# Optimization experiments

Measured on AMD Instinct MI355X. Metric: run time of the kernel, lower is better.

The kernel has to match this reference:

```python
import jax, jax.numpy as jnp
import numpy as np

B, U, D, SKIP = 2048, 1024, 1024, 24

def setup_inputs() -> dict:
    key = jax.random.key(0)
    ks = jax.random.split(key, 8)
    return {
        "inputs": jax.random.normal(ks[0], (B, D), dtype=jnp.float32),
        "h_tm1": jax.random.normal(ks[1], (B, 4 * U), dtype=jnp.float32),
        "c_tm1": jax.random.normal(ks[2], (B, U), dtype=jnp.float32),
        "step": jnp.zeros((B, 1), dtype=jnp.float32),
        "prev_h": jax.random.normal(ks[3], (B, U * SKIP), dtype=jnp.float32),
        "kernel": jax.random.normal(ks[4], (D, 4 * U), dtype=jnp.float32) * (1.0 / np.sqrt(D)),
        "recurrent_kernel": jax.random.normal(ks[5], (U, 4 * U), dtype=jnp.float32) * (1.0 / np.sqrt(U)),
        "kernel2": jax.random.normal(ks[6], (U, U), dtype=jnp.float32) * (1.0 / np.sqrt(U)),
        "bias": jnp.zeros((4 * U,), dtype=jnp.float32),
        "bias2": jnp.zeros((U,), dtype=jnp.float32),
        "s0": jnp.float32(0.5),
    }

def reference(inputs, h_tm1, c_tm1, step, prev_h, kernel, recurrent_kernel, kernel2, bias, bias2, s0):
    units = kernel2.shape[0]
    # split previous 'h' state into its four gate-history blocks [B, U] each
    h_parts = jnp.stack(jnp.split(h_tm1, 4, axis=1), axis=0)          # [4, B, U]
    rk = recurrent_kernel.reshape(units, 4, units)                     # [U, 4, U]
    # fused per-gate recurrent matmuls: r[g] = h_parts[g] @ recurrent_kernel[:, g*U:(g+1)*U]
    r = jnp.einsum('gbu,ugv->gbv', h_parts, rk)                        # [4, B, U]
    x = inputs @ kernel + bias                                         # [B, 4U]
    x_i, x_f, x_c, x_o = jnp.split(x, 4, axis=1)
    i = jax.nn.sigmoid(x_i + r[0])
    f = jax.nn.sigmoid(x_f + r[1])
    c = f * c_tm1 + i * jnp.tanh(x_c + r[2])
    o = jax.nn.sigmoid(x_o + r[3])
    h = o * jnp.tanh(c)
    new_h_skip = jax.nn.sigmoid(prev_h[:, :units] @ kernel2 + bias2)
    h = s0 * h + new_h_skip * (1 - s0)
    new_h_tm1 = jnp.concatenate([i, f, c, o], axis=1)
    new_prev_h = jnp.concatenate([prev_h[:, units:], h], axis=1)
    return (h, new_h_tm1, c, step + 1, new_prev_h)
```

## Files before the change

kernel.cpp:

```cpp
#include <hip/hip_runtime.h>
#include <hip/hip_bf16.h>
#include <stdint.h>

#define BB 2048
#define UU 1024
#define SKIPN 24

typedef __attribute__((ext_vector_type(8))) short short8;
typedef __attribute__((ext_vector_type(4))) float f32x4;
typedef __attribute__((ext_vector_type(4))) unsigned short ushort4_t;

static __device__ __forceinline__ float sigmoidf_(float x) {
    return 1.0f / (1.0f + __expf(-x));
}

static __device__ __forceinline__ void load_lds16(const void* g, void* l) {
    __builtin_amdgcn_global_load_lds((const __attribute__((address_space(1))) void*)g,
                                     (__attribute__((address_space(3))) void*)l, 16, 0, 0);
}

static __device__ __forceinline__ f32x4 ntl(const f32x4* p) {
    return __builtin_nontemporal_load(p);
}
static __device__ __forceinline__ void nts(f32x4* p, f32x4 v) {
    __builtin_nontemporal_store(v, p);
}

__global__ __launch_bounds__(256) void prep(
    const float* __restrict__ inputs, const float* __restrict__ h_tm1,
    const float* __restrict__ prev_h, const float* __restrict__ kernel,
    const float* __restrict__ rkernel, const float* __restrict__ kernel2,
    __hip_bfloat16* __restrict__ kt, __hip_bfloat16* __restrict__ rkt,
    __hip_bfloat16* __restrict__ k2t, __hip_bfloat16* __restrict__ xin,
    __hip_bfloat16* __restrict__ hb, __hip_bfloat16* __restrict__ ph0) {
    const int bid = blockIdx.x;
    if (bid < 9216) {
        __shared__ float tile[32][33];
        const float* src;
        __hip_bfloat16* dst;
        int C, local;
        if (bid < 4096)      { src = kernel;  dst = kt;  C = 4096; local = bid; }
        else if (bid < 8192) { src = rkernel; dst = rkt; C = 4096; local = bid - 4096; }
        else                 { src = kernel2; dst = k2t; C = 1024; local = bid - 8192; }
        const int xt = (C == 4096) ? 128 : 32;
        const int bc = (local % xt) * 32;
        const int br = (local / xt) * 32;
        const int tx = threadIdx.x & 31, ty = threadIdx.x >> 5;
#pragma unroll
        for (int i = 0; i < 32; i += 8)
            tile[ty + i][tx] = src[(size_t)(br + ty + i) * C + bc + tx];
        __syncthreads();
#pragma unroll
        for (int i = 0; i < 32; i += 8)
            dst[(size_t)(bc + ty + i) * 1024 + br + tx] = __float2bfloat16(tile[tx][ty + i]);
    } else {
        const int idx = (bid - 9216) * 256 + threadIdx.x;
        const float* src;
        __hip_bfloat16* dst;
        int off;
        if (idx < 524288) { dst = xin; off = idx; src = inputs + (size_t)off * 4; }
        else if (idx < 2621440) { off = idx - 524288; dst = hb; src = h_tm1 + (size_t)off * 4; }
        else {
            const int i = idx - 2621440;
            const int b = i >> 8, c4 = i & 255;
            off = i; dst = ph0;
            src = prev_h + (size_t)b * (UU * SKIPN) + c4 * 4;
        }
        const float4 v = *(const float4*)src;
        union { __hip_bfloat16 h[4]; ushort4_t u; } cv;
        cv.h[0] = __float2bfloat16(v.x);
        cv.h[1] = __float2bfloat16(v.y);
        cv.h[2] = __float2bfloat16(v.z);
        cv.h[3] = __float2bfloat16(v.w);
        *(ushort4_t*)(dst + (size_t)off * 4) = cv.u;
    }
}

__global__ __launch_bounds__(256) void mega6(
    const __hip_bfloat16* __restrict__ xin,
    const __hip_bfloat16* __restrict__ hb,
    const __hip_bfloat16* __restrict__ ph0,
    const __hip_bfloat16* __restrict__ kt,
    const __hip_bfloat16* __restrict__ rkt,
    const __hip_bfloat16* __restrict__ k2t,
    const float* __restrict__ prev_h, float* __restrict__ out_prev,
    __hip_bfloat16* __restrict__ pre) {
    const int bid = blockIdx.x;
    if (bid >= 640) {
        const int b = bid - 640;
        const f32x4* s = (const f32x4*)(prev_h + (size_t)b * 24576 + 1024);
        f32x4* d = (f32x4*)(out_prev + (size_t)b * 24576);
        int c = threadIdx.x;
#pragma unroll 1
        for (int it = 0; it < 5; ++it) {
            f32x4 v0 = ntl(s + c);
            f32x4 v1 = ntl(s + c + 256);
            f32x4 v2 = ntl(s + c + 512);
            f32x4 v3 = ntl(s + c + 768);
            nts(d + c, v0);
            nts(d + c + 256, v1);
            nts(d + c + 512, v2);
            nts(d + c + 768, v3);
            c += 1024;
        }
        {
            f32x4 v0 = ntl(s + c);
            f32x4 v1 = ntl(s + c + 256);
            f32x4 v2 = ntl(s + c + 512);
            nts(d + c, v0);
            nts(d + c + 256, v1);
            nts(d + c + 512, v2);
        }
        return;
    }
    const int gi = bid;
    const int g = gi % 5;
    const int t = gi / 5;
    const int v0 = (t & 7) * 128;
    const int b0 = (t >> 3) * 128;

    __shared__ char As[3 * 8192];
    __shared__ char Bs[3 * 8192];

    const int tid = threadIdx.x;
    const int lane = tid & 63;
    const int wid = tid >> 6;
    const int wrow = wid >> 1;
    const int wcol = wid & 1;

    const int srow = tid >> 2;
    const int sslot = tid & 3;
    const int kofs = ((sslot ^ (srow & 3) ^ ((srow >> 2) & 3)) << 3);
    const int ldst = wid * 1024;

    const int l15 = lane & 15;
    const int hi = lane >> 4;
    const int rswB = ((hi ^ (l15 & 3) ^ ((l15 >> 2) & 3)) << 4);

    f32x4 acc[4][4];
#pragma unroll
    for (int m = 0; m < 4; m++)
#pragma unroll
        for (int n = 0; n < 4; n++) acc[m][n] = (f32x4){0.f, 0.f, 0.f, 0.f};

    const __hip_bfloat16* A1;
    const __hip_bfloat16* W1;
    const __hip_bfloat16* A2 = nullptr;
    const __hip_bfloat16* W2 = nullptr;
    int lda1;
    if (g < 4) {
        A1 = xin; lda1 = 1024;
        W1 = kt + (size_t)g * 1048576;
        A2 = hb + (size_t)g * 1024;
        W2 = rkt + (size_t)g * 1048576;
    } else {
        A1 = ph0; lda1 = 1024;
        W1 = k2t;
    }

#define BARRIER() asm volatile("s_barrier" ::: "memory")
#define WAITV(N) asm volatile("s_waitcnt vmcnt(" #N ")" ::: "memory")
#define WAITL0() asm volatile("s_waitcnt lgkmcnt(0)" ::: "memory")

#define KSEG(AB, LDA, WB)                                                          \
    {                                                                              \
        const __hip_bfloat16* Ar0 = (AB) + (size_t)(b0 + srow) * (LDA) + kofs;     \
        const __hip_bfloat16* Ar1 = (AB) + (size_t)(b0 + 64 + srow) * (LDA) + kofs;\
        const __hip_bfloat16* Wr0 = (WB) + (size_t)(v0 + srow) * 1024 + kofs;      \
        const __hip_bfloat16* Wr1 = (WB) + (size_t)(v0 + 64 + srow) * 1024 + kofs; \
        load_lds16(Ar0, As + ldst);                                                \
        load_lds16(Ar1, As + ldst + 4096);                                         \
        load_lds16(Wr0, Bs + ldst);                                                \
        load_lds16(Wr1, Bs + ldst + 4096);                                         \
        load_lds16(Ar0 + 32, As + 8192 + ldst);                                    \
        load_lds16(Ar1 + 32, As + 8192 + ldst + 4096);                             \
        load_lds16(Wr0 + 32, Bs + 8192 + ldst);                                    \
        load_lds16(Wr1 + 32, Bs + 8192 + ldst + 4096);                             \
        int cur = 0;                                                               \
        for (int t_ = 0; t_ < 32; ++t_) {                                          \
            char* Ac = As + cur * 8192;                                            \
            char* Bc = Bs + cur * 8192;                                            \
            if (t_ < 30) {                                                         \
                int nxt = cur + 2; if (nxt >= 3) nxt -= 3;                         \
                const int kn = (t_ + 2) * 32;                                      \
                char* An = As + nxt * 8192 + ldst;                                 \
                char* Bn = Bs + nxt * 8192 + ldst;                                 \
                load_lds16(Ar0 + kn, An);                                          \
                load_lds16(Ar1 + kn, An + 4096);                                   \
                load_lds16(Wr0 + kn, Bn);                                          \
                load_lds16(Wr1 + kn, Bn + 4096);                                   \
                WAITV(8);                                                          \
            } else if (t_ == 30) {                                                 \
                WAITV(4);                                                          \
            } else {                                                               \
                WAITV(0);                                                          \
            }                                                                      \
            BARRIER();                                                             \
            short8 af[4], bfr[4];                                                  \
            _Pragma("unroll")                                                      \
            for (int m = 0; m < 4; m++)                                            \
                af[m] = *(const short8*)(Ac + (wrow * 64 + m * 16 + l15) * 64 + rswB); \
            _Pragma("unroll")                                                      \
            for (int n = 0; n < 4; n++)                                            \
                bfr[n] = *(const short8*)(Bc + (wcol * 64 + n * 16 + l15) * 64 + rswB); \
            __builtin_amdgcn_s_setprio(1);                                         \
            _Pragma("unroll")                                                      \
            for (int m = 0; m < 4; m++)                                            \
                _Pragma("unroll")                                                  \
                for (int n = 0; n < 4; n++)                                        \
                    acc[m][n] = __builtin_amdgcn_mfma_f32_16x16x32_bf16(af[m], bfr[n], acc[m][n], 0, 0, 0); \
            __builtin_amdgcn_s_setprio(0);                                         \
            WAITL0();                                                              \
            BARRIER();                                                             \
            cur = (cur == 2) ? 0 : cur + 1;                                        \
        }                                                                          \
    }

    KSEG(A1, lda1, W1);
    if (g < 4) KSEG(A2, 4096, W2);
#undef KSEG

    __hip_bfloat16* P = pre + (size_t)g * 2097152;
#pragma unroll
    for (int m = 0; m < 4; m++) {
#pragma unroll
        for (int n = 0; n < 4; n++) {
            const int col = v0 + wcol * 64 + n * 16 + l15;
            const int row = b0 + wrow * 64 + m * 16 + hi * 4;
#pragma unroll
            for (int r = 0; r < 4; r++)
                P[(size_t)(row + r) * 1024 + col] = __float2bfloat16(acc[m][n][r]);
        }
    }
#undef BARRIER
#undef WAITV
#undef WAITL0
}

__global__ __launch_bounds__(256) void epilogue3(
    const __hip_bfloat16* __restrict__ pre,
    const float* __restrict__ c_tm1, const float* __restrict__ bias,
    const float* __restrict__ bias2, const float* __restrict__ s0p,
    const float* __restrict__ step, float* __restrict__ out_h,
    float* __restrict__ out_ht, float* __restrict__ out_c,
    float* __restrict__ out_step, float* __restrict__ out_prev, int write_tail) {
    const int idx = blockIdx.x * 256 + threadIdx.x;
    const int b = idx >> 7;
    const int v = (idx & 127) * 8;
    const size_t bv = (size_t)b * 1024 + v;

    union u8 { short8 s; unsigned short u[8]; };
    u8 pi, pf, pc, po, ps;
    pi.s = *(const short8*)(pre + bv);
    pf.s = *(const short8*)(pre + 2097152 + bv);
    pc.s = *(const short8*)(pre + 4194304 + bv);
    po.s = *(const short8*)(pre + 6291456 + bv);
    ps.s = *(const short8*)(pre + 8388608 + bv);
    const float s0 = s0p[0];

    float hv[8], iv8[8], fv8[8], cn8[8], ov8[8];
#pragma unroll
    for (int j = 0; j < 8; j++) {
        const float pif = __bfloat162float(*(const __hip_bfloat16*)&pi.u[j]) + bias[v + j];
        const float pff = __bfloat162float(*(const __hip_bfloat16*)&pf.u[j]) + bias[1024 + v + j];
        const float pcf = __bfloat162float(*(const __hip_bfloat16*)&pc.u[j]) + bias[2048 + v + j];
        const float pof = __bfloat162float(*(const __hip_bfloat16*)&po.u[j]) + bias[3072 + v + j];
        const float psf = __bfloat162float(*(const __hip_bfloat16*)&ps.u[j]) + bias2[v + j];
        const float ct = c_tm1[bv + j];
        const float iv = sigmoidf_(pif);
        const float fv = sigmoidf_(pff);
        const float cn = fv * ct + iv * tanhf(pcf);
        const float ov = sigmoidf_(pof);
        const float sk = sigmoidf_(psf);
        hv[j] = s0 * (ov * tanhf(cn)) + sk * (1.0f - s0);
        iv8[j] = iv; fv8[j] = fv; cn8[j] = cn; ov8[j] = ov;
    }
#pragma unroll
    for (int q = 0; q < 2; q++) {
        const int o = q * 4;
        *(float4*)(out_h + bv + o) = make_float4(hv[o], hv[o+1], hv[o+2], hv[o+3]);
        *(float4*)(out_c + bv + o) = make_float4(cn8[o], cn8[o+1], cn8[o+2], cn8[o+3]);
        float* ht = out_ht + (size_t)b * 4096 + v + o;
        *(float4*)(ht) = make_float4(iv8[o], iv8[o+1], iv8[o+2], iv8[o+3]);
        *(float4*)(ht + 1024) = make_float4(fv8[o], fv8[o+1], fv8[o+2], fv8[o+3]);
        *(float4*)(ht + 2048) = make_float4(cn8[o], cn8[o+1], cn8[o+2], cn8[o+3]);
        *(float4*)(ht + 3072) = make_float4(ov8[o], ov8[o+1], ov8[o+2], ov8[o+3]);
        if (write_tail)
            *(float4*)(out_prev + (size_t)b * 24576 + 23552 + v + o) =
                make_float4(hv[o], hv[o+1], hv[o+2], hv[o+3]);
    }
    if (idx < 2048) out_step[idx] = step[idx] + 1.0f;
}

__global__ __launch_bounds__(256) void shift_only(
    const float* __restrict__ prev_h, const float* __restrict__ out_h,
    float* __restrict__ out_prev) {
    const int b = blockIdx.x;
    float4* d = (float4*)(out_prev + (size_t)b * 24576);
    const float4* s1 = (const float4*)(prev_h + (size_t)b * 24576 + 1024);
    const float4* s2 = (const float4*)(out_h + (size_t)b * 1024);
    for (int c = threadIdx.x; c < 6144; c += 256)
        d[c] = (c < 5888) ? s1[c] : s2[c - 5888];
}

extern "C" void kernel_launch(void* const* d_in, const int* in_sizes, int n_in,
                              void* d_out, int out_size, void* d_ws, size_t ws_size,
                              hipStream_t stream) {
    (void)in_sizes; (void)n_in; (void)out_size;
    const float* inputs = (const float*)d_in[0];
    const float* h_tm1 = (const float*)d_in[1];
    const float* c_tm1 = (const float*)d_in[2];
    const float* step = (const float*)d_in[3];
    const float* prev_h = (const float*)d_in[4];
    const float* kernel = (const float*)d_in[5];
    const float* rkernel = (const float*)d_in[6];
    const float* kernel2 = (const float*)d_in[7];
    const float* bias = (const float*)d_in[8];
    const float* bias2 = (const float*)d_in[9];
    const float* s0 = (const float*)d_in[10];

    float* out = (float*)d_out;
    float* out_h = out;
    float* out_ht = out + 2097152;
    float* out_c = out + 10485760;
    float* out_step = out + 12582912;
    float* out_prev = out + 12584960;

    const size_t NEED = 44040192 + 20971520;
    const int fits = (ws_size >= NEED);
    char* scr = fits ? (char*)d_ws : (char*)out_prev;
    __hip_bfloat16* kt = (__hip_bfloat16*)(scr + 0);
    __hip_bfloat16* rkt = (__hip_bfloat16*)(scr + 8388608);
    __hip_bfloat16* k2t = (__hip_bfloat16*)(scr + 16777216);
    __hip_bfloat16* xin = (__hip_bfloat16*)(scr + 18874368);
    __hip_bfloat16* hb = (__hip_bfloat16*)(scr + 23068672);
    __hip_bfloat16* ph0 = (__hip_bfloat16*)(scr + 39845888);
    __hip_bfloat16* pre = (__hip_bfloat16*)(scr + 44040192);

    prep<<<21504, 256, 0, stream>>>(inputs, h_tm1, prev_h, kernel, rkernel, kernel2,
                                    kt, rkt, k2t, xin, hb, ph0);
    if (fits) {
        mega6<<<2688, 256, 0, stream>>>(xin, hb, ph0, kt, rkt, k2t, prev_h, out_prev, pre);
        epilogue3<<<1024, 256, 0, stream>>>(pre, c_tm1, bias, bias2, s0, step,
                                            out_h, out_ht, out_c, out_step, out_prev, 1);
    } else {
        mega6<<<640, 256, 0, stream>>>(xin, hb, ph0, kt, rkt, k2t, prev_h, out_prev, pre);
        epilogue3<<<1024, 256, 0, stream>>>(pre, c_tm1, bias, bias2, s0, step,
                                            out_h, out_ht, out_c, out_step, out_prev, 0);
        shift_only<<<2048, 256, 0, stream>>>(prev_h, out_h, out_prev);
    }
}
```

Baseline: 162.5 us.

## Fold prev_h shift copy into GEMM blocks via extra barrier-synced copy warps

The 2048 standalone copy blocks that shifted prev_h are gone. Each of the 640 GEMM blocks now runs 384 threads, and the extra 128 threads perform that block's share of the shift copy. The copy threads step through the same number of s_barrier calls as the K-loop iterations (64 for gate blocks, 32 for the skip block), so the copy traffic is spread across the matmul main loop. This is meant to hide the memory-bound copy behind compute. In exchange it makes the blocks larger, which may reduce occupancy, and it depends on the barrier counts of the two thread groups matching exactly.

```diff
diff --git a/kernel.cpp b/kernel.cpp
--- a/kernel.cpp
+++ b/kernel.cpp
@@ -76,7 +76,11 @@
     }
 }
 
-__global__ __launch_bounds__(256) void mega6(
+#define BARRIER() asm volatile("s_barrier" ::: "memory")
+#define WAITV(N) asm volatile("s_waitcnt vmcnt(" #N ")" ::: "memory")
+#define WAITL0() asm volatile("s_waitcnt lgkmcnt(0)" ::: "memory")
+
+__global__ __launch_bounds__(384) void mega7(
     const __hip_bfloat16* __restrict__ xin,
     const __hip_bfloat16* __restrict__ hb,
     const __hip_bfloat16* __restrict__ ph0,
@@ -85,37 +89,56 @@
     const __hip_bfloat16* __restrict__ k2t,
     const float* __restrict__ prev_h, float* __restrict__ out_prev,
     __hip_bfloat16* __restrict__ pre) {
-    const int bid = blockIdx.x;
-    if (bid >= 640) {
-        const int b = bid - 640;
-        const f32x4* s = (const f32x4*)(prev_h + (size_t)b * 24576 + 1024);
-        f32x4* d = (f32x4*)(out_prev + (size_t)b * 24576);
-        int c = threadIdx.x;
-#pragma unroll 1
-        for (int it = 0; it < 5; ++it) {
-            f32x4 v0 = ntl(s + c);
-            f32x4 v1 = ntl(s + c + 256);
-            f32x4 v2 = ntl(s + c + 512);
-            f32x4 v3 = ntl(s + c + 768);
-            nts(d + c, v0);
-            nts(d + c + 256, v1);
-            nts(d + c + 512, v2);
-            nts(d + c + 768, v3);
-            c += 1024;
-        }
-        {
-            f32x4 v0 = ntl(s + c);
-            f32x4 v1 = ntl(s + c + 256);
-            f32x4 v2 = ntl(s + c + 512);
-            nts(d + c, v0);
-            nts(d + c + 256, v1);
-            nts(d + c + 512, v2);
+    const int gi = blockIdx.x;
+    const int g = gi % 5;
+    const int t = gi / 5;
+    const int NB = (g < 4) ? 64 : 32;
+
+    if (threadIdx.x >= 256) {
+        const int ct = threadIdx.x - 256;
+        const int nr = (gi < 128) ? 4 : 3;
+        const int total = nr * 46;
+        const int CH = (total + NB - 1) / NB;
+        const f32x4* sb = (const f32x4*)prev_h;
+        f32x4* db = (f32x4*)out_prev;
+        for (int it = 0; it < NB; ++it) {
+            const int js = it * CH;
+            const int je = (js + CH < total) ? (js + CH) : total;
+            f32x4 v0, v1, v2, v3, v4, v5;
+            size_t s0_ = 0, s1_ = 0, s2_ = 0, s3_ = 0, s4_ = 0, s5_ = 0;
+            bool k0 = false, k1 = false, k2 = false, k3 = false, k4 = false, k5 = false;
+#define CLOAD(K, VK, SK, OK)                                                     \
+            {                                                                    \
+                const int q = js + K;                                            \
+                OK = (K < CH) && (q < je);                                       \
+                if (OK) {                                                        \
+                    const int ri = q / 46;                                       \
+                    const int pc = q - ri * 46;                                  \
+                    const int rr = gi + ri * 640;                                \
+                    const int col = ct + pc * 128;                               \
+                    SK = (size_t)rr * 6144 + col;                                \
+                    VK = ntl(sb + SK + 256);                                     \
+                }                                                                \
+            }
+            CLOAD(0, v0, s0_, k0)
+            CLOAD(1, v1, s1_, k1)
+            CLOAD(2, v2, s2_, k2)
+            CLOAD(3, v3, s3_, k3)
+            CLOAD(4, v4, s4_, k4)
+            CLOAD(5, v5, s5_, k5)
+#undef CLOAD
+            BARRIER();
+            if (k0) nts(db + s0_, v0);
+            if (k1) nts(db + s1_, v1);
+            if (k2) nts(db + s2_, v2);
+            if (k3) nts(db + s3_, v3);
+            if (k4) nts(db + s4_, v4);
+            if (k5) nts(db + s5_, v5);
+            BARRIER();
         }
         return;
     }
-    const int gi = bid;
-    const int g = gi % 5;
-    const int t = gi / 5;
+
     const int v0 = (t & 7) * 128;
     const int b0 = (t >> 3) * 128;
 
@@ -157,10 +180,6 @@
         A1 = ph0; lda1 = 1024;
         W1 = k2t;
     }
-
-#define BARRIER() asm volatile("s_barrier" ::: "memory")
-#define WAITV(N) asm volatile("s_waitcnt vmcnt(" #N ")" ::: "memory")
-#define WAITL0() asm volatile("s_waitcnt lgkmcnt(0)" ::: "memory")
 
 #define KSEG(AB, LDA, WB)                                                          \
     {                                                                              \
@@ -232,9 +251,6 @@
                 P[(size_t)(row + r) * 1024 + col] = __float2bfloat16(acc[m][n][r]);
         }
     }
-#undef BARRIER
-#undef WAITV
-#undef WAITL0
 }
 
 __global__ __launch_bounds__(256) void epilogue3(
@@ -340,11 +356,11 @@
     prep<<<21504, 256, 0, stream>>>(inputs, h_tm1, prev_h, kernel, rkernel, kernel2,
                                     kt, rkt, k2t, xin, hb, ph0);
     if (fits) {
-        mega6<<<2688, 256, 0, stream>>>(xin, hb, ph0, kt, rkt, k2t, prev_h, out_prev, pre);
+        mega7<<<640, 384, 0, stream>>>(xin, hb, ph0, kt, rkt, k2t, prev_h, out_prev, pre);
         epilogue3<<<1024, 256, 0, stream>>>(pre, c_tm1, bias, bias2, s0, step,
                                             out_h, out_ht, out_c, out_step, out_prev, 1);
     } else {
-        mega6<<<640, 256, 0, stream>>>(xin, hb, ph0, kt, rkt, k2t, prev_h, out_prev, pre);
+        mega7<<<640, 256, 0, stream>>>(xin, hb, ph0, kt, rkt, k2t, prev_h, out_prev, pre);
         epilogue3<<<1024, 256, 0, stream>>>(pre, c_tm1, bias, bias2, s0, step,
                                             out_h, out_ht, out_c, out_step, out_prev, 0);
         shift_only<<<2048, 256, 0, stream>>>(prev_h, out_h, out_prev);
```

New measurement: 364.3 us. +124.1%, slower.

## Fuse LSTM epilogue into GEMM kernel via last-arriver atomic counter per tile

Applied to the files above, without the earlier changes.

The separate epilogue launch is folded into the GEMM kernel. Each of the five gate GEMM blocks for a given output tile bumps an atomic counter after writing its bf16 pre-activations, and the last block to arrive runs the elementwise LSTM/skip epilogue for that 128x128 tile. The aim is to drop one kernel launch and the pass that re-reads pre-activations from memory. In exchange it adds a memset launch, threadfences, and a serial epilogue tail on the winning blocks, which reduces parallelism for that phase.

```diff
diff --git a/kernel.cpp b/kernel.cpp
--- a/kernel.cpp
+++ b/kernel.cpp
@@ -76,7 +76,11 @@
     }
 }
 
-__global__ __launch_bounds__(256) void mega6(
+#define BARRIER() asm volatile("s_barrier" ::: "memory")
+#define WAITV(N) asm volatile("s_waitcnt vmcnt(" #N ")" ::: "memory")
+#define WAITL0() asm volatile("s_waitcnt lgkmcnt(0)" ::: "memory")
+
+__global__ __launch_bounds__(256) void mega8(
     const __hip_bfloat16* __restrict__ xin,
     const __hip_bfloat16* __restrict__ hb,
     const __hip_bfloat16* __restrict__ ph0,
@@ -84,7 +88,13 @@
     const __hip_bfloat16* __restrict__ rkt,
     const __hip_bfloat16* __restrict__ k2t,
     const float* __restrict__ prev_h, float* __restrict__ out_prev,
-    __hip_bfloat16* __restrict__ pre) {
+    __hip_bfloat16* __restrict__ pre,
+    unsigned int* __restrict__ cnt,
+    const float* __restrict__ c_tm1, const float* __restrict__ bias,
+    const float* __restrict__ bias2, const float* __restrict__ s0p,
+    const float* __restrict__ step, float* __restrict__ out_h,
+    float* __restrict__ out_ht, float* __restrict__ out_c,
+    float* __restrict__ out_step) {
     const int bid = blockIdx.x;
     if (bid >= 640) {
         const int b = bid - 640;
@@ -121,6 +131,7 @@
 
     __shared__ char As[3 * 8192];
     __shared__ char Bs[3 * 8192];
+    __shared__ unsigned int winflag;
 
     const int tid = threadIdx.x;
     const int lane = tid & 63;
@@ -157,10 +168,6 @@
         A1 = ph0; lda1 = 1024;
         W1 = k2t;
     }
-
-#define BARRIER() asm volatile("s_barrier" ::: "memory")
-#define WAITV(N) asm volatile("s_waitcnt vmcnt(" #N ")" ::: "memory")
-#define WAITL0() asm volatile("s_waitcnt lgkmcnt(0)" ::: "memory")
 
 #define KSEG(AB, LDA, WB)                                                          \
     {                                                                              \
@@ -232,23 +239,74 @@
                 P[(size_t)(row + r) * 1024 + col] = __float2bfloat16(acc[m][n][r]);
         }
     }
-#undef BARRIER
-#undef WAITV
-#undef WAITL0
+
+    if (!cnt) return;
+    __threadfence();
+    __syncthreads();
+    if (tid == 0) winflag = atomicAdd(&cnt[t], 1u);
+    __syncthreads();
+    if (winflag != 4u) return;
+    __threadfence();
+
+    const float s0 = s0p[0];
+    for (int i = tid; i < 2048; i += 256) {
+        const int b = b0 + (i >> 4);
+        const int v = v0 + (i & 15) * 8;
+        const size_t bv = (size_t)b * 1024 + v;
+        union u8 { short8 s; unsigned short u[8]; };
+        u8 pi, pf, pc, po, ps;
+        pi.s = *(const short8*)(pre + bv);
+        pf.s = *(const short8*)(pre + 2097152 + bv);
+        pc.s = *(const short8*)(pre + 4194304 + bv);
+        po.s = *(const short8*)(pre + 6291456 + bv);
+        ps.s = *(const short8*)(pre + 8388608 + bv);
+        float hv[8], iv8[8], fv8[8], cn8[8], ov8[8];
+#pragma unroll
+        for (int j = 0; j < 8; j++) {
+            const float pif = __bfloat162float(*(const __hip_bfloat16*)&pi.u[j]) + bias[v + j];
+            const float pff = __bfloat162float(*(const __hip_bfloat16*)&pf.u[j]) + bias[1024 + v + j];
+            const float pcf = __bfloat162float(*(const __hip_bfloat16*)&pc.u[j]) + bias[2048 + v + j];
+            const float pof = __bfloat162float(*(const __hip_bfloat16*)&po.u[j]) + bias[3072 + v + j];
+            const float psf = __bfloat162float(*(const __hip_bfloat16*)&ps.u[j]) + bias2[v + j];
+            const float ct = c_tm1[bv + j];
+            const float iv = sigmoidf_(pif);
+            const float fv = sigmoidf_(pff);
+            const float cn = fv * ct + iv * tanhf(pcf);
+            const float ov = sigmoidf_(pof);
+            const float sk = sigmoidf_(psf);
+            hv[j] = s0 * (ov * tanhf(cn)) + sk * (1.0f - s0);
+            iv8[j] = iv; fv8[j] = fv; cn8[j] = cn; ov8[j] = ov;
+        }
+#pragma unroll
+        for (int q = 0; q < 2; q++) {
+            const int o = q * 4;
+            *(float4*)(out_h + bv + o) = make_float4(hv[o], hv[o+1], hv[o+2], hv[o+3]);
+            *(float4*)(out_c + bv + o) = make_float4(cn8[o], cn8[o+1], cn8[o+2], cn8[o+3]);
+            float* ht = out_ht + (size_t)b * 4096 + v + o;
+            *(float4*)(ht) = make_float4(iv8[o], iv8[o+1], iv8[o+2], iv8[o+3]);
+            *(float4*)(ht + 1024) = make_float4(fv8[o], fv8[o+1], fv8[o+2], fv8[o+3]);
+            *(float4*)(ht + 2048) = make_float4(cn8[o], cn8[o+1], cn8[o+2], cn8[o+3]);
+            *(float4*)(ht + 3072) = make_float4(ov8[o], ov8[o+1], ov8[o+2], ov8[o+3]);
+            *(float4*)(out_prev + (size_t)b * 24576 + 23552 + v + o) =
+                make_float4(hv[o], hv[o+1], hv[o+2], hv[o+3]);
+        }
+    }
+    if ((t & 7) == 0 && tid < 128) {
+        const int b = b0 + tid;
+        out_step[b] = step[b] + 1.0f;
+    }
 }
 
 __global__ __launch_bounds__(256) void epilogue3(
-    const __hip_bfloat16* __restrict__ pre,
-    const float* __restrict__ c_tm1, const float* __restrict__ bias,
-    const float* __restrict__ bias2, const float* __restrict__ s0p,
-    const float* __restrict__ step, float* __restrict__ out_h,
-    float* __restrict__ out_ht, float* __restrict__ out_c,
-    float* __restrict__ out_step, float* __restrict__ out_prev, int write_tail) {
+    const __hip_bfloat16* __restrict__ pre, const float* __restrict__ c_tm1,
+    const float* __restrict__ bias, const float* __restrict__ bias2,
+    const float* __restrict__ s0p, const float* __restrict__ step,
+    float* __restrict__ out_h, float* __restrict__ out_ht,
+    float* __restrict__ out_c, float* __restrict__ out_step) {
     const int idx = blockIdx.x * 256 + threadIdx.x;
     const int b = idx >> 7;
     const int v = (idx & 127) * 8;
     const size_t bv = (size_t)b * 1024 + v;
-
     union u8 { short8 s; unsigned short u[8]; };
     u8 pi, pf, pc, po, ps;
     pi.s = *(const short8*)(pre + bv);
@@ -257,7 +315,6 @@
     po.s = *(const short8*)(pre + 6291456 + bv);
     ps.s = *(const short8*)(pre + 8388608 + bv);
     const float s0 = s0p[0];
-
     float hv[8], iv8[8], fv8[8], cn8[8], ov8[8];
 #pragma unroll
     for (int j = 0; j < 8; j++) {
@@ -285,9 +342,6 @@
         *(float4*)(ht + 1024) = make_float4(fv8[o], fv8[o+1], fv8[o+2], fv8[o+3]);
         *(float4*)(ht + 2048) = make_float4(cn8[o], cn8[o+1], cn8[o+2], cn8[o+3]);
         *(float4*)(ht + 3072) = make_float4(ov8[o], ov8[o+1], ov8[o+2], ov8[o+3]);
-        if (write_tail)
-            *(float4*)(out_prev + (size_t)b * 24576 + 23552 + v + o) =
-                make_float4(hv[o], hv[o+1], hv[o+2], hv[o+3]);
     }
     if (idx < 2048) out_step[idx] = step[idx] + 1.0f;
 }
@@ -326,7 +380,7 @@
     float* out_step = out + 12582912;
     float* out_prev = out + 12584960;
 
-    const size_t NEED = 44040192 + 20971520;
+    const size_t NEED = 44040192 + 20971520 + 512;
     const int fits = (ws_size >= NEED);
     char* scr = fits ? (char*)d_ws : (char*)out_prev;
     __hip_bfloat16* kt = (__hip_bfloat16*)(scr + 0);
@@ -336,17 +390,21 @@
     __hip_bfloat16* hb = (__hip_bfloat16*)(scr + 23068672);
     __hip_bfloat16* ph0 = (__hip_bfloat16*)(scr + 39845888);
     __hip_bfloat16* pre = (__hip_bfloat16*)(scr + 44040192);
+    unsigned int* cnt = (unsigned int*)(scr + 65011712);
 
     prep<<<21504, 256, 0, stream>>>(inputs, h_tm1, prev_h, kernel, rkernel, kernel2,
                                     kt, rkt, k2t, xin, hb, ph0);
     if (fits) {
-        mega6<<<2688, 256, 0, stream>>>(xin, hb, ph0, kt, rkt, k2t, prev_h, out_prev, pre);
+        hipMemsetAsync(cnt, 0, 512, stream);
+        mega8<<<2688, 256, 0, stream>>>(xin, hb, ph0, kt, rkt, k2t, prev_h, out_prev,
+                                        pre, cnt, c_tm1, bias, bias2, s0, step,
+                                        out_h, out_ht, out_c, out_step);
+    } else {
+        mega8<<<640, 256, 0, stream>>>(xin, hb, ph0, kt, rkt, k2t, prev_h, out_prev,
+                                       pre, nullptr, c_tm1, bias, bias2, s0, step,
+                                       out_h, out_ht, out_c, out_step);
         epilogue3<<<1024, 256, 0, stream>>>(pre, c_tm1, bias, bias2, s0, step,
-                                            out_h, out_ht, out_c, out_step, out_prev, 1);
-    } else {
-        mega6<<<640, 256, 0, stream>>>(xin, hb, ph0, kt, rkt, k2t, prev_h, out_prev, pre);
-        epilogue3<<<1024, 256, 0, stream>>>(pre, c_tm1, bias, bias2, s0, step,
-                                            out_h, out_ht, out_c, out_step, out_prev, 0);
+                                            out_h, out_ht, out_c, out_step);
         shift_only<<<2048, 256, 0, stream>>>(prev_h, out_h, out_prev);
     }
 }
```

After: 365.0 us. 125% more time.
